# Optimization experiments

Hardware: AMD Instinct MI355X
Metric: run time of the kernel (lower is better)

## Reference

```python
import jax, jax.numpy as jnp
import numpy as np

EPS = 1e-5
K = 5

def _bn(x, g, b):
    # BatchNorm1d in training mode: biased batch statistics
    mu = jnp.mean(x, axis=0)
    var = jnp.mean((x - mu) ** 2, axis=0)
    return (x - mu) * jax.lax.rsqrt(var + EPS) * g + b

def setup_inputs():
    key = jax.random.key(0)
    ks = jax.random.split(key, 16)
    N, M, D, F = 16384, 8192, 512, 2048
    s = 0.02
    return dict(
        src=jax.random.normal(ks[0], (N, D), jnp.float32),
        anchor_2=jax.random.normal(ks[1], (M, D), jnp.float32),
        W_dim=jax.random.normal(ks[2], (D, D), jnp.float32) * s,
        b_dim=jnp.zeros((D,), jnp.float32),
        W_fus=jax.random.normal(ks[3], (2 * D, D), jnp.float32) * s,
        b_fus=jnp.zeros((D,), jnp.float32),
        W_e1=jax.random.normal(ks[4], (D, F), jnp.float32) * s,
        b_e1=jnp.zeros((F,), jnp.float32),
        W_e2=jax.random.normal(ks[5], (F, D), jnp.float32) * s,
        b_e2=jnp.zeros((D,), jnp.float32),
        g1=jnp.ones((D,), jnp.float32), bt1=jnp.zeros((D,), jnp.float32),
        g2=jnp.ones((D,), jnp.float32), bt2=jnp.zeros((D,), jnp.float32),
        W_d=jax.random.normal(ks[6], (D, D), jnp.float32) * s,
        b_d=jnp.zeros((D,), jnp.float32),
        g_d=jnp.ones((D,), jnp.float32), bt_d=jnp.zeros((D,), jnp.float32),
    )

def reference(src, anchor_2, W_dim, b_dim, W_fus, b_fus, W_e1, b_e1, W_e2, b_e2,
              g1, bt1, g2, bt2, W_d, b_d, g_d, bt_d):
    # kNN in Euclidean metric (sklearn NearestNeighbors): squared distances suffice
    # d2[n,m] = ||src_n||^2 - 2 src_n . a_m + ||a_m||^2   -> [N, M]
    d2 = (jnp.sum(src * src, axis=1, keepdims=True)
          - 2.0 * (src @ anchor_2.T)
          + jnp.sum(anchor_2 * anchor_2, axis=1)[None, :])
    _, idx = jax.lax.top_k(-d2, K)                      # [N, K] nearest anchors
    neigh = jnp.mean(anchor_2[idx], axis=1)             # gather + mean -> [N, D]
    a_map = neigh @ W_dim + b_dim                       # linear_dim
    comb = jnp.concatenate([src, a_map], axis=1) @ W_fus + b_fus
    comb = _bn(comb, g1, bt1)                           # norm1
    # encoder MLP (dropout is identity in eval)
    t = jnp.tanh(comb @ W_e1 + b_e1) @ W_e2 + b_e2
    comb = _bn(comb + t, g2, bt2)                       # residual + norm2
    out = jnp.tanh(_bn(comb @ W_d + b_d, g_d, bt_d))    # decoder
    return out
```

## Files before the change

### kernel.cpp

```cpp
#include <hip/hip_runtime.h>
#include <math.h>

#define N_ROWS 16384
#define M_ANCH 8192
#define DDIM   512
#define FDIM   2048
#define KNN    5
#define BN_EPS 1e-5f
#define CHUNK  8192
#define SEED   1024
#define CAND_MAX 256
#define MARGIN 6.0f
#define QSCALE 28.0f
#define TWO_INV_S2 (2.0f / (QSCALE * QSCALE))

typedef _Float16 f16;
typedef _Float16 f16x8 __attribute__((ext_vector_type(8)));
typedef _Float16 f16x4 __attribute__((ext_vector_type(4)));
typedef float f32x4 __attribute__((ext_vector_type(4)));
typedef int   i32x4 __attribute__((ext_vector_type(4)));

__device__ __forceinline__ void async_copy16(const void* g, void* l) {
    __builtin_amdgcn_global_load_lds(
        (const __attribute__((address_space(1))) void*)g,
        (__attribute__((address_space(3))) void*)l, 16, 0, 0);
}

__device__ __forceinline__ bool kless(float k1, int i1, float k2, int i2) {
    return (k1 < k2) || (k1 == k2 && i1 < i2);
}

__device__ __forceinline__ void insert5(float (&bk)[KNN], int (&bi)[KNN], float key, int id) {
    if (!kless(key, id, bk[4], bi[4])) return;
    bool c3 = kless(key, id, bk[3], bi[3]);
    bool c2 = kless(key, id, bk[2], bi[2]);
    bool c1 = kless(key, id, bk[1], bi[1]);
    bool c0 = kless(key, id, bk[0], bi[0]);
    bk[4] = c3 ? bk[3] : key;                  bi[4] = c3 ? bi[3] : id;
    bk[3] = c3 ? (c2 ? bk[2] : key) : bk[3];   bi[3] = c3 ? (c2 ? bi[2] : id) : bi[3];
    bk[2] = c2 ? (c1 ? bk[1] : key) : bk[2];   bi[2] = c2 ? (c1 ? bi[1] : id) : bi[2];
    bk[1] = c1 ? (c0 ? bk[0] : key) : bk[1];   bi[1] = c1 ? (c0 ? bi[0] : id) : bi[1];
    bk[0] = c0 ? key : bk[0];                  bi[0] = c0 ? id : bi[0];
}

__global__ void zero_kernel(float* p, int n) {
    int i = blockIdx.x * blockDim.x + threadIdx.x;
    if (i < n) p[i] = 0.f;
}

__global__ __launch_bounds__(256) void quant_i8_kernel(const float* __restrict__ X,
                                                       unsigned int* __restrict__ Y, int n4) {
    int i = blockIdx.x * 256 + threadIdx.x;
    if (i >= n4) return;
    float4 v = ((const float4*)X)[i];
    int a = (int)rintf(v.x * QSCALE); a = a > 127 ? 127 : (a < -127 ? -127 : a);
    int b = (int)rintf(v.y * QSCALE); b = b > 127 ? 127 : (b < -127 ? -127 : b);
    int c = (int)rintf(v.z * QSCALE); c = c > 127 ? 127 : (c < -127 ? -127 : c);
    int d = (int)rintf(v.w * QSCALE); d = d > 127 ? 127 : (d < -127 ? -127 : d);
    Y[i] = (unsigned int)(a & 255) | ((unsigned int)(b & 255) << 8)
         | ((unsigned int)(c & 255) << 16) | ((unsigned int)(d & 255) << 24);
}

__global__ __launch_bounds__(256) void anchor_norm_kernel(const float* __restrict__ a,
                                                          float* __restrict__ norm_a) {
    int wave = threadIdx.x >> 6, lane = threadIdx.x & 63;
    int row = blockIdx.x * 4 + wave;
    const float4* ar = (const float4*)(a + (size_t)row * DDIM);
    float4 v1 = ar[lane * 2];
    float4 v2 = ar[lane * 2 + 1];
    float s = v1.x*v1.x + v1.y*v1.y + v1.z*v1.z + v1.w*v1.w
            + v2.x*v2.x + v2.y*v2.y + v2.z*v2.z + v2.w*v2.w;
    for (int off = 32; off; off >>= 1) s += __shfl_xor(s, off, 64);
    if (lane == 0) norm_a[row] = s;
}

template<int COLLECT>
__global__ __launch_bounds__(256) void gemm_i8(
    const char* __restrict__ A, const char* __restrict__ B,
    const float* __restrict__ norm, const float* __restrict__ thr,
    int* __restrict__ cnt, int* __restrict__ cand_i, float* __restrict__ cand_n,
    int idofs, float* __restrict__ C, int Ncols)
{
    __shared__ char As[2][128 * 64];
    __shared__ char Bs[2][128 * 64];
    const int t = threadIdx.x;
    const int w = t >> 6, l = t & 63;
    const int m0 = blockIdx.y * 128, n0 = blockIdx.x * 128;
    const int wm = (w & 1) * 64, wn = (w >> 1) * 64;

    i32x4 acc[4][4];
    #pragma unroll
    for (int i = 0; i < 4; ++i)
        #pragma unroll
        for (int j = 0; j < 4; ++j) acc[i][j] = (i32x4){0, 0, 0, 0};

    const int srow = l >> 2;
    const int gq = ((l & 3) - (srow >> 1)) & 3;
    const int skoff = gq * 16;
    const int sqf = (((l >> 4) + (((l & 15) >> 1) & 3)) & 3) * 16;

    auto STAGE = [&](int buf, int kt) {
        int k0 = kt * 64;
        #pragma unroll
        for (int s = 0; s < 2; ++s) {
            int grp = w * 2 + s;
            int row = grp * 16 + srow;
            async_copy16(A + (size_t)(m0 + row) * DDIM + k0 + skoff,
                         &As[buf][grp * 1024 + l * 16]);
            async_copy16(B + (size_t)(n0 + row) * DDIM + k0 + skoff,
                         &Bs[buf][grp * 1024 + l * 16]);
        }
    };

    STAGE(0, 0);
    __syncthreads();

    for (int kt = 0; kt < 8; ++kt) {
        int cur = kt & 1;
        if (kt < 7) STAGE(cur ^ 1, kt + 1);
        i32x4 af[4], bf[4];
        #pragma unroll
        for (int i = 0; i < 4; ++i)
            af[i] = *(const i32x4*)&As[cur][(wm + i * 16 + (l & 15)) * 64 + sqf];
        #pragma unroll
        for (int j = 0; j < 4; ++j)
            bf[j] = *(const i32x4*)&Bs[cur][(wn + j * 16 + (l & 15)) * 64 + sqf];
        #pragma unroll
        for (int i = 0; i < 4; ++i)
            #pragma unroll
            for (int j = 0; j < 4; ++j)
                acc[i][j] = __builtin_amdgcn_mfma_i32_16x16x64_i8(af[i], bf[j], acc[i][j], 0, 0, 0);
        __syncthreads();
    }

    float nj[4];
    #pragma unroll
    for (int j = 0; j < 4; ++j) nj[j] = norm[n0 + wn + j * 16 + (l & 15)];

    if (COLLECT) {
        float thr4[4][4];
        #pragma unroll
        for (int i = 0; i < 4; ++i) {
            float4 tv = *(const float4*)&thr[m0 + wm + i * 16 + (l >> 4) * 4];
            thr4[i][0] = tv.x; thr4[i][1] = tv.y; thr4[i][2] = tv.z; thr4[i][3] = tv.w;
        }
        #pragma unroll
        for (int i = 0; i < 4; ++i)
            #pragma unroll
            for (int j = 0; j < 4; ++j)
                #pragma unroll
                for (int r = 0; r < 4; ++r) {
                    float key = nj[j] - TWO_INV_S2 * (float)acc[i][j][r];
                    if (key < thr4[i][r]) {
                        int row = m0 + wm + i * 16 + (l >> 4) * 4 + r;
                        int pos = atomicAdd(&cnt[row], 1);
                        if (pos < CAND_MAX) {
                            cand_i[(size_t)row * CAND_MAX + pos] =
                                idofs + n0 + wn + j * 16 + (l & 15);
                            cand_n[(size_t)row * CAND_MAX + pos] = nj[j];
                        }
                    }
                }
    } else {
        #pragma unroll
        for (int i = 0; i < 4; ++i)
            #pragma unroll
            for (int j = 0; j < 4; ++j)
                #pragma unroll
                for (int r = 0; r < 4; ++r) {
                    int m = m0 + wm + i * 16 + (l >> 4) * 4 + r;
                    int n = n0 + wn + j * 16 + (l & 15);
                    C[(size_t)m * Ncols + n] = nj[j] - TWO_INV_S2 * (float)acc[i][j][r];
                }
    }
}

__global__ __launch_bounds__(256) void topk_scan_kernel(
    const float* __restrict__ g, const float* __restrict__ norm_a,
    float* __restrict__ thrbuf, int* __restrict__ cnt,
    int* __restrict__ cand_i, float* __restrict__ cand_n)
{
    int row = blockIdx.x * 4 + (threadIdx.x >> 6);
    int lane = threadIdx.x & 63;
    const float* grow = g + (size_t)row * SEED;
    float4 v0 = *(const float4*)(grow + lane * 4);
    float4 v1 = *(const float4*)(grow + 256 + lane * 4);
    float4 v2 = *(const float4*)(grow + 512 + lane * 4);
    float4 v3 = *(const float4*)(grow + 768 + lane * 4);
    float bk[KNN]; int bi[KNN];
    #pragma unroll
    for (int q = 0; q < KNN; ++q) { bk[q] = 3.0e38f; bi[q] = 0x7fffffff; }
    int c = lane * 4;
    insert5(bk, bi, v0.x, c);       insert5(bk, bi, v0.y, c + 1);
    insert5(bk, bi, v0.z, c + 2);   insert5(bk, bi, v0.w, c + 3);
    insert5(bk, bi, v1.x, c + 256); insert5(bk, bi, v1.y, c + 257);
    insert5(bk, bi, v1.z, c + 258); insert5(bk, bi, v1.w, c + 259);
    insert5(bk, bi, v2.x, c + 512); insert5(bk, bi, v2.y, c + 513);
    insert5(bk, bi, v2.z, c + 514); insert5(bk, bi, v2.w, c + 515);
    insert5(bk, bi, v3.x, c + 768); insert5(bk, bi, v3.y, c + 769);
    insert5(bk, bi, v3.z, c + 770); insert5(bk, bi, v3.w, c + 771);
    for (int off = 32; off >= 1; off >>= 1) {
        float ok[KNN]; int oi[KNN];
        #pragma unroll
        for (int q = 0; q < KNN; ++q) {
            ok[q] = __shfl_xor(bk[q], off, 64);
            oi[q] = __shfl_xor(bi[q], off, 64);
        }
        #pragma unroll
        for (int q = 0; q < KNN; ++q) insert5(bk, bi, ok[q], oi[q]);
    }
    float thr = bk[4] + MARGIN;
    if (lane == 0) thrbuf[row] = thr;
    int* rci = cand_i + (size_t)row * CAND_MAX;
    float* rcn = cand_n + (size_t)row * CAND_MAX;
    #define PUSH(v, id) if ((v) < thr) { int pos = atomicAdd(&cnt[row], 1); \
                                         if (pos < CAND_MAX) { rci[pos] = (id); \
                                         rcn[pos] = norm_a[(id)]; } }
    PUSH(v0.x, c)       PUSH(v0.y, c + 1)   PUSH(v0.z, c + 2)   PUSH(v0.w, c + 3)
    PUSH(v1.x, c + 256) PUSH(v1.y, c + 257) PUSH(v1.z, c + 258) PUSH(v1.w, c + 259)
    PUSH(v2.x, c + 512) PUSH(v2.y, c + 513) PUSH(v2.z, c + 514) PUSH(v2.w, c + 515)
    PUSH(v3.x, c + 768) PUSH(v3.y, c + 769) PUSH(v3.z, c + 770) PUSH(v3.w, c + 771)
    #undef PUSH
}

__global__ __launch_bounds__(256) void rescore_kernel(
    const float* __restrict__ src, const float* __restrict__ anchor,
    const int* __restrict__ cnt, const int* __restrict__ cand_i,
    const float* __restrict__ cand_n, float* __restrict__ neigh)
{
    __shared__ float lb[4][2][DDIM];
    int wv = threadIdx.x >> 6, lane = threadIdx.x & 63;
    int row = blockIdx.x * 4 + wv;
    const float4* sp = (const float4*)(src + (size_t)row * DDIM);
    float4 s0 = sp[lane * 2], s1 = sp[lane * 2 + 1];
    int c = cnt[row]; if (c > CAND_MAX) c = CAND_MAX;
    const int* ci = cand_i + (size_t)row * CAND_MAX;
    const float* cn = cand_n + (size_t)row * CAND_MAX;

    float bk[KNN]; int bi[KNN];
    #pragma unroll
    for (int q = 0; q < KNN; ++q) { bk[q] = 3.0e38f; bi[q] = 0x7fffffff; }

    auto PREF = [&](int buf, int id) {
        const float* gp = anchor + (size_t)id * DDIM;
        async_copy16(gp + lane * 4, &lb[wv][buf][lane * 4]);
        async_copy16(gp + 256 + lane * 4, &lb[wv][buf][256 + lane * 4]);
    };

    int   id_c = ci[0];          float n_c = cn[0];
    int   id_n = ci[1];          float n_n = cn[1];
    PREF(0, id_c);
    PREF(1, id_n);

    for (int p = 0; p < c; ++p) {
        int id_f = 0; float n_f = 0.f;
        if (p + 2 < c) { id_f = ci[p + 2]; n_f = cn[p + 2]; }
        asm volatile("s_waitcnt vmcnt(4)" ::: "memory");
        const float* bc = &lb[wv][p & 1][0];
        float4 a0 = *(const float4*)&bc[lane * 8];
        float4 a1 = *(const float4*)&bc[lane * 8 + 4];
        float d = s0.x*a0.x + s0.y*a0.y + s0.z*a0.z + s0.w*a0.w
                + s1.x*a1.x + s1.y*a1.y + s1.z*a1.z + s1.w*a1.w;
        #pragma unroll
        for (int off = 32; off; off >>= 1) d += __shfl_xor(d, off, 64);
        insert5(bk, bi, n_c - 2.f * d, id_c);
        if (p + 2 < c) PREF(p & 1, id_f);
        id_c = id_n; n_c = n_n;
        id_n = id_f; n_n = n_f;
    }

    const float4* a0 = (const float4*)(anchor + (size_t)bi[0] * DDIM);
    const float4* a1 = (const float4*)(anchor + (size_t)bi[1] * DDIM);
    const float4* a2 = (const float4*)(anchor + (size_t)bi[2] * DDIM);
    const float4* a3 = (const float4*)(anchor + (size_t)bi[3] * DDIM);
    const float4* a4 = (const float4*)(anchor + (size_t)bi[4] * DDIM);
    float4* np = (float4*)(neigh + (size_t)row * DDIM);
    #pragma unroll
    for (int p = 0; p < 2; ++p) {
        int c4 = lane + 64 * p;
        float4 v0 = a0[c4], v1 = a1[c4], v2 = a2[c4], v3 = a3[c4], v4 = a4[c4];
        float4 o;
        o.x = (v0.x + v1.x + v2.x + v3.x + v4.x) * 0.2f;
        o.y = (v0.y + v1.y + v2.y + v3.y + v4.y) * 0.2f;
        o.z = (v0.z + v1.z + v2.z + v3.z + v4.z) * 0.2f;
        o.w = (v0.w + v1.w + v2.w + v3.w + v4.w) * 0.2f;
        np[c4] = o;
    }
}

template<int ADDC0, int TANH, int K>
__global__ __launch_bounds__(256) void gemm_split_nt(
    const float* __restrict__ A, const f16* __restrict__ Bw,
    const float* __restrict__ bias, const float* __restrict__ C0,
    float* __restrict__ C, int Ncols)
{
    __shared__ f16 Ah[128 * 32];
    __shared__ f16 Al[128 * 32];
    __shared__ f16 Bh[128 * 32];
    __shared__ f16 Bl[128 * 32];
    const int t = threadIdx.x;
    const int w = t >> 6, l = t & 63;
    const int m0 = blockIdx.y * 128, n0 = blockIdx.x * 128;
    const int wm = (w & 1) * 64, wn = (w >> 1) * 64;
    const int K2 = 2 * K;

    f32x4 acc[4][4];
    #pragma unroll
    for (int i = 0; i < 4; ++i)
        #pragma unroll
        for (int j = 0; j < 4; ++j) acc[i][j] = (f32x4){0.f, 0.f, 0.f, 0.f};

    const int ar = t >> 1;
    const int ac = (t & 1) * 16;
    const int arq = (ar >> 1) & 3;
    const int s0 = (((t & 1) * 2 + 0 + arq) & 3) * 8;
    const int s1 = (((t & 1) * 2 + 1 + arq) & 3) * 8;
    const int srow = l >> 2;
    const int gq = ((l & 3) - (srow >> 1)) & 3;
    const int skoff = gq * 8;
    const int sqf = (((l >> 4) + (((l & 15) >> 1) & 3)) & 3) * 8;

    for (int k0 = 0; k0 < K; k0 += 32) {
        __syncthreads();
        #pragma unroll
        for (int s = 0; s < 2; ++s) {
            int grp = w * 2 + s;
            int row = grp * 16 + srow;
            const f16* bp = Bw + (size_t)(n0 + row) * K2 + k0 + skoff;
            async_copy16(bp, Bh + grp * 512 + l * 8);
            async_copy16(bp + K, Bl + grp * 512 + l * 8);
        }
        {
            const float* ap = A + (size_t)(m0 + ar) * K + k0 + ac;
            float xs[16];
            *(float4*)&xs[0]  = *(const float4*)ap;
            *(float4*)&xs[4]  = *(const float4*)(ap + 4);
            *(float4*)&xs[8]  = *(const float4*)(ap + 8);
            *(float4*)&xs[12] = *(const float4*)(ap + 12);
            f16x8 h0, h1, lo0, lo1;
            #pragma unroll
            for (int e = 0; e < 8; ++e) {
                f16 hh = (f16)xs[e];
                h0[e] = hh; lo0[e] = (f16)(xs[e] - (float)hh);
                f16 hh2 = (f16)xs[8 + e];
                h1[e] = hh2; lo1[e] = (f16)(xs[8 + e] - (float)hh2);
            }
            *(f16x8*)&Ah[ar * 32 + s0] = h0;  *(f16x8*)&Ah[ar * 32 + s1] = h1;
            *(f16x8*)&Al[ar * 32 + s0] = lo0; *(f16x8*)&Al[ar * 32 + s1] = lo1;
        }
        __syncthreads();
        f16x8 afh[4], afl[4], bfh[4], bfl[4];
        #pragma unroll
        for (int i = 0; i < 4; ++i) {
            int base = (wm + i * 16 + (l & 15)) * 32 + sqf;
            afh[i] = *(const f16x8*)(Ah + base);
            afl[i] = *(const f16x8*)(Al + base);
        }
        #pragma unroll
        for (int j = 0; j < 4; ++j) {
            int base = (wn + j * 16 + (l & 15)) * 32 + sqf;
            bfh[j] = *(const f16x8*)(Bh + base);
            bfl[j] = *(const f16x8*)(Bl + base);
        }
        #pragma unroll
        for (int i = 0; i < 4; ++i)
            #pragma unroll
            for (int j = 0; j < 4; ++j) {
                acc[i][j] = __builtin_amdgcn_mfma_f32_16x16x32_f16(afh[i], bfh[j], acc[i][j], 0, 0, 0);
                acc[i][j] = __builtin_amdgcn_mfma_f32_16x16x32_f16(afl[i], bfh[j], acc[i][j], 0, 0, 0);
                acc[i][j] = __builtin_amdgcn_mfma_f32_16x16x32_f16(afh[i], bfl[j], acc[i][j], 0, 0, 0);
            }
    }
    float bv[4];
    #pragma unroll
    for (int j = 0; j < 4; ++j)
        bv[j] = bias ? bias[n0 + wn + j * 16 + (l & 15)] : 0.f;
    #pragma unroll
    for (int i = 0; i < 4; ++i)
        #pragma unroll
        for (int j = 0; j < 4; ++j)
            #pragma unroll
            for (int r = 0; r < 4; ++r) {
                int m = m0 + wm + i * 16 + (l >> 4) * 4 + r;
                int n = n0 + wn + j * 16 + (l & 15);
                float v = acc[i][j][r] + bv[j];
                if (ADDC0) v += C0[(size_t)m * Ncols + n];
                if (TANH)  v = tanhf(v);
                C[(size_t)m * Ncols + n] = v;
            }
}

__global__ __launch_bounds__(256) void wsplit_kernel(const float* __restrict__ W,
                                                     f16* __restrict__ Wt,
                                                     int K, int N)
{
    __shared__ float tile[64][65];
    const int t = threadIdx.x;
    const int kb = blockIdx.y * 64, nb = blockIdx.x * 64;
    #pragma unroll
    for (int i = 0; i < 4; ++i) {
        int r = (t >> 4) + i * 16;
        int c = (t & 15) * 4;
        *(float4*)&tile[r][c] = *(const float4*)&W[(size_t)(kb + r) * N + nb + c];
    }
    __syncthreads();
    const int r2 = t >> 2;
    const int kc = (t & 3) * 16;
    f16x8 h0, h1, lo0, lo1;
    #pragma unroll
    for (int e = 0; e < 8; ++e) {
        float x = tile[kc + e][r2];
        f16 hh = (f16)x; h0[e] = hh; lo0[e] = (f16)(x - (float)hh);
        float y = tile[kc + 8 + e][r2];
        f16 hh2 = (f16)y; h1[e] = hh2; lo1[e] = (f16)(y - (float)hh2);
    }
    f16* base = Wt + (size_t)(nb + r2) * 2 * K + kb + kc;
    *(f16x8*)base = h0; *(f16x8*)(base + 8) = h1;
    *(f16x8*)(base + K) = lo0; *(f16x8*)(base + K + 8) = lo1;
}

__global__ __launch_bounds__(256) void bcomb_kernel(const float* __restrict__ b_dim,
                                                    const float* __restrict__ W_fus2,
                                                    const float* __restrict__ b_fus,
                                                    float* __restrict__ b_comb)
{
    int n = blockIdx.x * 256 + threadIdx.x;
    if (n >= DDIM) return;
    float s = b_fus[n];
    for (int k = 0; k < DDIM; ++k) s += b_dim[k] * W_fus2[(size_t)k * DDIM + n];
    b_comb[n] = s;
}

template<int ACT>
__global__ __launch_bounds__(256) void gemm_kernel(
    const float* __restrict__ A, int K1,
    const float* __restrict__ A2, int K2,
    const float* __restrict__ B, const float* __restrict__ bias,
    float* __restrict__ C, int Ncols)
{
    __shared__ float As[16][132];
    __shared__ float Bs[16][128];
    const int t = threadIdx.x;
    const int n0 = blockIdx.x * 128;
    const int m0 = blockIdx.y * 128;
    const int ty = t >> 4, tx = t & 15;
    const int K = K1 + K2;

    float acc[8][8];
    #pragma unroll
    for (int i = 0; i < 8; ++i)
        #pragma unroll
        for (int j = 0; j < 8; ++j) acc[i][j] = 0.f;

    const int ar = t >> 1;
    const int akc = (t & 1) * 8;
    const int bkr = t >> 4;
    const int bc = (t & 15) * 8;

    for (int k0 = 0; k0 < K; k0 += 16) {
        int kk = k0 + akc;
        float4 v0, v1;
        if (kk < K1) {
            const float* p = A + (size_t)(m0 + ar) * K1 + kk;
            v0 = *(const float4*)p; v1 = *(const float4*)(p + 4);
        } else {
            const float* p = A2 + (size_t)(m0 + ar) * K2 + (kk - K1);
            v0 = *(const float4*)p; v1 = *(const float4*)(p + 4);
        }
        const float* bp = B + (size_t)(k0 + bkr) * Ncols + n0 + bc;
        float4 w0 = *(const float4*)bp, w1 = *(const float4*)(bp + 4);
        __syncthreads();
        As[akc+0][ar] = v0.x; As[akc+1][ar] = v0.y; As[akc+2][ar] = v0.z; As[akc+3][ar] = v0.w;
        As[akc+4][ar] = v1.x; As[akc+5][ar] = v1.y; As[akc+6][ar] = v1.z; As[akc+7][ar] = v1.w;
        *(float4*)&Bs[bkr][bc] = w0; *(float4*)&Bs[bkr][bc + 4] = w1;
        __syncthreads();
        #pragma unroll
        for (int k = 0; k < 16; ++k) {
            float a[8], b[8];
            *(float4*)&a[0] = *(const float4*)&As[k][ty * 8];
            *(float4*)&a[4] = *(const float4*)&As[k][ty * 8 + 4];
            *(float4*)&b[0] = *(const float4*)&Bs[k][tx * 4];
            *(float4*)&b[4] = *(const float4*)&Bs[k][64 + tx * 4];
            #pragma unroll
            for (int i = 0; i < 8; ++i)
                #pragma unroll
                for (int j = 0; j < 8; ++j) acc[i][j] += a[i] * b[j];
        }
    }
    float4 bv0 = *(const float4*)(bias + n0 + tx * 4);
    float4 bv1 = *(const float4*)(bias + n0 + 64 + tx * 4);
    #pragma unroll
    for (int i = 0; i < 8; ++i) {
        int row = m0 + ty * 8 + i;
        float4 o0, o1;
        o0.x = acc[i][0] + bv0.x; o0.y = acc[i][1] + bv0.y;
        o0.z = acc[i][2] + bv0.z; o0.w = acc[i][3] + bv0.w;
        o1.x = acc[i][4] + bv1.x; o1.y = acc[i][5] + bv1.y;
        o1.z = acc[i][6] + bv1.z; o1.w = acc[i][7] + bv1.w;
        if (ACT == 1) {
            o0.x = tanhf(o0.x); o0.y = tanhf(o0.y); o0.z = tanhf(o0.z); o0.w = tanhf(o0.w);
            o1.x = tanhf(o1.x); o1.y = tanhf(o1.y); o1.z = tanhf(o1.z); o1.w = tanhf(o1.w);
        }
        *(float4*)(C + (size_t)row * Ncols + n0 + tx * 4) = o0;
        *(float4*)(C + (size_t)row * Ncols + n0 + 64 + tx * 4) = o1;
    }
}

__global__ __launch_bounds__(256) void bn_stats_kernel(const float* __restrict__ X,
                                                       float* __restrict__ sums)
{
    __shared__ float red[8][64];
    int lane = threadIdx.x & 63;
    int rl = threadIdx.x >> 6;
    int c = blockIdx.x * 64 + lane;
    int chunk = N_ROWS / gridDim.y;
    int rbeg = blockIdx.y * chunk;
    float s = 0.f, s2 = 0.f;
    for (int r = rbeg + rl; r < rbeg + chunk; r += 4) {
        float v = X[(size_t)r * DDIM + c];
        s += v; s2 += v * v;
    }
    red[rl][lane] = s; red[4 + rl][lane] = s2;
    __syncthreads();
    if (threadIdx.x < 64) {
        float ts = red[0][lane] + red[1][lane] + red[2][lane] + red[3][lane];
        float t2 = red[4][lane] + red[5][lane] + red[6][lane] + red[7][lane];
        atomicAdd(&sums[c], ts);
        atomicAdd(&sums[DDIM + c], t2);
    }
}

template<int TANH>
__global__ __launch_bounds__(256) void bn_apply_kernel(
    const float* __restrict__ X, float* __restrict__ Y,
    const float* __restrict__ sums, const float* __restrict__ g,
    const float* __restrict__ b, float invN)
{
    size_t i = (size_t)blockIdx.x * 256 + threadIdx.x;
    int cg = (int)(i % (DDIM / 4));
    int c = cg * 4;
    float4 x = ((const float4*)X)[i];
    float4 sm = *(const float4*)(sums + c);
    float4 sq = *(const float4*)(sums + DDIM + c);
    float4 gv = *(const float4*)(g + c);
    float4 bv = *(const float4*)(b + c);
    float m, var, rs;
    m = sm.x * invN; var = sq.x * invN - m * m; rs = rsqrtf(var + BN_EPS);
    x.x = (x.x - m) * rs * gv.x + bv.x;
    m = sm.y * invN; var = sq.y * invN - m * m; rs = rsqrtf(var + BN_EPS);
    x.y = (x.y - m) * rs * gv.y + bv.y;
    m = sm.z * invN; var = sq.z * invN - m * m; rs = rsqrtf(var + BN_EPS);
    x.z = (x.z - m) * rs * gv.z + bv.z;
    m = sm.w * invN; var = sq.w * invN - m * m; rs = rsqrtf(var + BN_EPS);
    x.w = (x.w - m) * rs * gv.w + bv.w;
    if (TANH) { x.x = tanhf(x.x); x.y = tanhf(x.y); x.z = tanhf(x.z); x.w = tanhf(x.w); }
    ((float4*)Y)[i] = x;
}

extern "C" void kernel_launch(void* const* d_in, const int* in_sizes, int n_in,
                              void* d_out, int out_size, void* d_ws, size_t ws_size,
                              hipStream_t stream)
{
    const float* src   = (const float*)d_in[0];
    const float* anc   = (const float*)d_in[1];
    const float* W_dim = (const float*)d_in[2];
    const float* b_dim = (const float*)d_in[3];
    const float* W_fus = (const float*)d_in[4];
    const float* b_fus = (const float*)d_in[5];
    const float* W_e1  = (const float*)d_in[6];
    const float* b_e1  = (const float*)d_in[7];
    const float* W_e2  = (const float*)d_in[8];
    const float* b_e2  = (const float*)d_in[9];
    const float* g1    = (const float*)d_in[10];
    const float* bt1   = (const float*)d_in[11];
    const float* g2    = (const float*)d_in[12];
    const float* bt2   = (const float*)d_in[13];
    const float* W_d   = (const float*)d_in[14];
    const float* b_d   = (const float*)d_in[15];
    const float* g_d   = (const float*)d_in[16];
    const float* bt_d  = (const float*)d_in[17];
    float* out = (float*)d_out;

    float* ws = (float*)d_ws;
    float* score  = ws;
    float* bufA   = ws + 16777216;
    char*  src2q  = (char*)(ws + 25165824);
    char*  anc2q  = (char*)(ws + 37748736);
    f16*   wbase  = (f16*)(ws + 25165824);
    f16*   Wt_fus1  = wbase;
    f16*   Wt_comb2 = wbase + 524288;
    f16*   Wt_e1    = wbase + 1048576;
    f16*   Wt_e2    = wbase + 3145728;
    f16*   Wt_d     = wbase + 5242880;
    float* cand_n   = ws + 29360128;
    float* W_comb2  = ws + 44040192;
    float* norm_a   = ws + 44302336;
    float* sums1    = ws + 44310528;
    float* sums2    = sums1 + 1024;
    float* sums3    = sums2 + 1024;
    float* zeros512 = ws + 44313600;
    float* b_comb   = ws + 44314112;
    float* thrbuf   = ws + 44478464;
    int*   cnt      = (int*)(ws + 44494848);
    int*   cand_i   = (int*)(ws + 48705536);

    const float invN = 1.0f / (float)N_ROWS;
    float* hbuf = score;

    zero_kernel<<<dim3(14), 256, 0, stream>>>(sums1, 3584);
    zero_kernel<<<dim3(64), 256, 0, stream>>>((float*)cnt, 16384);
    quant_i8_kernel<<<dim3(N_ROWS * DDIM / 1024), 256, 0, stream>>>(
        src, (unsigned int*)src2q, N_ROWS * DDIM / 4);
    quant_i8_kernel<<<dim3(M_ANCH * DDIM / 1024), 256, 0, stream>>>(
        anc, (unsigned int*)anc2q, M_ANCH * DDIM / 4);
    anchor_norm_kernel<<<dim3(M_ANCH / 4), 256, 0, stream>>>(anc, norm_a);

    gemm_i8<0><<<dim3(SEED / 128, N_ROWS / 128), 256, 0, stream>>>(
        src2q, anc2q, norm_a, nullptr, nullptr, nullptr, nullptr, 0, score, SEED);
    topk_scan_kernel<<<dim3(N_ROWS / 4), 256, 0, stream>>>(
        score, norm_a, thrbuf, cnt, cand_i, cand_n);
    gemm_i8<1><<<dim3((M_ANCH - SEED) / 128, N_ROWS / 128), 256, 0, stream>>>(
        src2q, anc2q + (size_t)SEED * DDIM, norm_a + SEED, thrbuf,
        cnt, cand_i, cand_n, SEED, nullptr, 0);
    rescore_kernel<<<dim3(N_ROWS / 4), 256, 0, stream>>>(
        src, anc, cnt, cand_i, cand_n, bufA);

    wsplit_kernel<<<dim3(DDIM / 64, DDIM / 64), 256, 0, stream>>>(W_fus, Wt_fus1, DDIM, DDIM);
    wsplit_kernel<<<dim3(FDIM / 64, DDIM / 64), 256, 0, stream>>>(W_e1, Wt_e1, DDIM, FDIM);
    wsplit_kernel<<<dim3(DDIM / 64, FDIM / 64), 256, 0, stream>>>(W_e2, Wt_e2, FDIM, DDIM);
    wsplit_kernel<<<dim3(DDIM / 64, DDIM / 64), 256, 0, stream>>>(W_d, Wt_d, DDIM, DDIM);
    gemm_kernel<0><<<dim3(4, 4), 256, 0, stream>>>(
        W_dim, DDIM, nullptr, 0, W_fus + DDIM * DDIM, zeros512, W_comb2, DDIM);
    bcomb_kernel<<<dim3(2), 256, 0, stream>>>(b_dim, W_fus + DDIM * DDIM, b_fus, b_comb);
    wsplit_kernel<<<dim3(DDIM / 64, DDIM / 64), 256, 0, stream>>>(W_comb2, Wt_comb2, DDIM, DDIM);

    gemm_split_nt<0, 0, DDIM><<<dim3(DDIM / 128, N_ROWS / 128), 256, 0, stream>>>(
        src, Wt_fus1, b_comb, nullptr, out, DDIM);
    gemm_split_nt<1, 0, DDIM><<<dim3(DDIM / 128, N_ROWS / 128), 256, 0, stream>>>(
        bufA, Wt_comb2, nullptr, out, out, DDIM);
    bn_stats_kernel<<<dim3(DDIM / 64, 16), 256, 0, stream>>>(out, sums1);
    bn_apply_kernel<0><<<dim3(8192), 256, 0, stream>>>(out, out, sums1, g1, bt1, invN);

    for (int r0 = 0; r0 < N_ROWS; r0 += CHUNK) {
        gemm_split_nt<0, 1, DDIM><<<dim3(FDIM / 128, CHUNK / 128), 256, 0, stream>>>(
            out + (size_t)r0 * DDIM, Wt_e1, b_e1, nullptr, hbuf, FDIM);
        gemm_split_nt<1, 0, FDIM><<<dim3(DDIM / 128, CHUNK / 128), 256, 0, stream>>>(
            hbuf, Wt_e2, b_e2, out + (size_t)r0 * DDIM, bufA + (size_t)r0 * DDIM,
            DDIM);
    }
    bn_stats_kernel<<<dim3(DDIM / 64, 16), 256, 0, stream>>>(bufA, sums2);
    bn_apply_kernel<0><<<dim3(8192), 256, 0, stream>>>(bufA, bufA, sums2, g2, bt2, invN);

    gemm_split_nt<0, 0, DDIM><<<dim3(DDIM / 128, N_ROWS / 128), 256, 0, stream>>>(
        bufA, Wt_d, b_d, nullptr, out, DDIM);
    bn_stats_kernel<<<dim3(DDIM / 64, 16), 256, 0, stream>>>(out, sums3);
    bn_apply_kernel<1><<<dim3(8192), 256, 0, stream>>>(out, out, sums3, g_d, bt_d, invN);
}
```

Before: 1.644 ms.

## Split kNN rescore across two waves per row and double-buffer split GEMM

The rescore kernel now assigns two wavefronts to each row, each scoring alternate candidates, then merges their top-5 lists through shared memory before one wave gathers and averages the neighbours. The split-fp16 GEMM gains double-buffered LDS tiles, so the next K-slice's A and B loads overlap the MFMA work on the current slice and one barrier per iteration is removed. The aim is more parallelism in the latency-bound candidate loop and better overlap of memory with compute in the GEMMs. The cost is doubled LDS use in the GEMM, which may lower occupancy, plus an extra block-level sync and an idle half of the waves during the rescore gather.

Result: slower. 1.690 ms (+2.8%).

```diff
diff --git a/kernel.cpp b/kernel.cpp
--- a/kernel.cpp
+++ b/kernel.cpp
@@ -229,13 +229,17 @@
     const float* __restrict__ cand_n, float* __restrict__ neigh)
 {
     __shared__ float lb[4][2][DDIM];
+    __shared__ float mgk[4][KNN];
+    __shared__ int   mgi[4][KNN];
     int wv = threadIdx.x >> 6, lane = threadIdx.x & 63;
-    int row = blockIdx.x * 4 + wv;
+    int row = blockIdx.x * 2 + (wv >> 1);
+    int sub = wv & 1;
     const float4* sp = (const float4*)(src + (size_t)row * DDIM);
     float4 s0 = sp[lane * 2], s1 = sp[lane * 2 + 1];
     int c = cnt[row]; if (c > CAND_MAX) c = CAND_MAX;
     const int* ci = cand_i + (size_t)row * CAND_MAX;
     const float* cn = cand_n + (size_t)row * CAND_MAX;
+    int nw = (c - sub + 1) >> 1;
 
     float bk[KNN]; int bi[KNN];
     #pragma unroll
@@ -243,48 +247,59 @@
 
     auto PREF = [&](int buf, int id) {
         const float* gp = anchor + (size_t)id * DDIM;
-        async_copy16(gp + lane * 4, &lb[wv][buf][lane * 4]);
-        async_copy16(gp + 256 + lane * 4, &lb[wv][buf][256 + lane * 4]);
+        async_copy16(gp + lane * 8,     &lb[wv][buf][lane * 4]);
+        async_copy16(gp + lane * 8 + 4, &lb[wv][buf][256 + lane * 4]);
     };
 
-    int   id_c = ci[0];          float n_c = cn[0];
-    int   id_n = ci[1];          float n_n = cn[1];
+    int   id_c = ci[sub];       float n_c = cn[sub];
+    int   id_n = ci[sub + 2];   float n_n = cn[sub + 2];
     PREF(0, id_c);
     PREF(1, id_n);
 
-    for (int p = 0; p < c; ++p) {
+    for (int t = 0; t < nw; ++t) {
         int id_f = 0; float n_f = 0.f;
-        if (p + 2 < c) { id_f = ci[p + 2]; n_f = cn[p + 2]; }
-        asm volatile("s_waitcnt vmcnt(4)" ::: "memory");
-        const float* bc = &lb[wv][p & 1][0];
-        float4 a0 = *(const float4*)&bc[lane * 8];
-        float4 a1 = *(const float4*)&bc[lane * 8 + 4];
+        if (t + 2 < nw) { id_f = ci[sub + 2 * (t + 2)]; n_f = cn[sub + 2 * (t + 2)]; }
+        if (t + 2 < nw)      asm volatile("s_waitcnt vmcnt(4)" ::: "memory");
+        else if (t + 1 < nw) asm volatile("s_waitcnt vmcnt(2)" ::: "memory");
+        else                 asm volatile("s_waitcnt vmcnt(0)" ::: "memory");
+        const float* bc = &lb[wv][t & 1][0];
+        float4 a0 = *(const float4*)&bc[lane * 4];
+        float4 a1 = *(const float4*)&bc[256 + lane * 4];
         float d = s0.x*a0.x + s0.y*a0.y + s0.z*a0.z + s0.w*a0.w
                 + s1.x*a1.x + s1.y*a1.y + s1.z*a1.z + s1.w*a1.w;
         #pragma unroll
         for (int off = 32; off; off >>= 1) d += __shfl_xor(d, off, 64);
         insert5(bk, bi, n_c - 2.f * d, id_c);
-        if (p + 2 < c) PREF(p & 1, id_f);
+        if (t + 2 < nw) PREF(t & 1, id_f);
         id_c = id_n; n_c = n_n;
         id_n = id_f; n_n = n_f;
     }
 
-    const float4* a0 = (const float4*)(anchor + (size_t)bi[0] * DDIM);
-    const float4* a1 = (const float4*)(anchor + (size_t)bi[1] * DDIM);
-    const float4* a2 = (const float4*)(anchor + (size_t)bi[2] * DDIM);
-    const float4* a3 = (const float4*)(anchor + (size_t)bi[3] * DDIM);
-    const float4* a4 = (const float4*)(anchor + (size_t)bi[4] * DDIM);
-    float4* np = (float4*)(neigh + (size_t)row * DDIM);
-    #pragma unroll
-    for (int p = 0; p < 2; ++p) {
-        int c4 = lane + 64 * p;
-        float4 v0 = a0[c4], v1 = a1[c4], v2 = a2[c4], v3 = a3[c4], v4 = a4[c4];
-        float4 o;
-        o.x = (v0.x + v1.x + v2.x + v3.x + v4.x) * 0.2f;
-        o.y = (v0.y + v1.y + v2.y + v3.y + v4.y) * 0.2f;
-        o.z = (v0.z + v1.z + v2.z + v3.z + v4.z) * 0.2f;
-        o.w = (v0.w + v1.w + v2.w + v3.w + v4.w) * 0.2f;
-        np[c4] = o;
+    if (lane == 0) {
+        #pragma unroll
+        for (int q = 0; q < KNN; ++q) { mgk[wv][q] = bk[q]; mgi[wv][q] = bi[q]; }
+    }
+    __syncthreads();
+    if (sub == 0) {
+        #pragma unroll
+        for (int q = 0; q < KNN; ++q) insert5(bk, bi, mgk[wv ^ 1][q], mgi[wv ^ 1][q]);
+        const float4* a0 = (const float4*)(anchor + (size_t)bi[0] * DDIM);
+        const float4* a1 = (const float4*)(anchor + (size_t)bi[1] * DDIM);
+        const float4* a2 = (const float4*)(anchor + (size_t)bi[2] * DDIM);
+        const float4* a3 = (const float4*)(anchor + (size_t)bi[3] * DDIM);
+        const float4* a4 = (const float4*)(anchor + (size_t)bi[4] * DDIM);
+        float4* np = (float4*)(neigh + (size_t)row * DDIM);
+        #pragma unroll
+        for (int p = 0; p < 2; ++p) {
+            int c4 = lane + 64 * p;
+            float4 v0 = a0[c4], v1 = a1[c4], v2 = a2[c4], v3 = a3[c4], v4 = a4[c4];
+            float4 o;
+            o.x = (v0.x + v1.x + v2.x + v3.x + v4.x) * 0.2f;
+            o.y = (v0.y + v1.y + v2.y + v3.y + v4.y) * 0.2f;
+            o.z = (v0.z + v1.z + v2.z + v3.z + v4.z) * 0.2f;
+            o.w = (v0.w + v1.w + v2.w + v3.w + v4.w) * 0.2f;
+            np[c4] = o;
+        }
     }
 }
 
@@ -294,15 +309,16 @@
     const float* __restrict__ bias, const float* __restrict__ C0,
     float* __restrict__ C, int Ncols)
 {
-    __shared__ f16 Ah[128 * 32];
-    __shared__ f16 Al[128 * 32];
-    __shared__ f16 Bh[128 * 32];
-    __shared__ f16 Bl[128 * 32];
+    __shared__ f16 Ah[2][128 * 32];
+    __shared__ f16 Al[2][128 * 32];
+    __shared__ f16 Bh[2][128 * 32];
+    __shared__ f16 Bl[2][128 * 32];
     const int t = threadIdx.x;
     const int w = t >> 6, l = t & 63;
     const int m0 = blockIdx.y * 128, n0 = blockIdx.x * 128;
     const int wm = (w & 1) * 64, wn = (w >> 1) * 64;
     const int K2 = 2 * K;
+    const int NK = K / 32;
 
     f32x4 acc[4][4];
     #pragma unroll
@@ -320,47 +336,62 @@
     const int skoff = gq * 8;
     const int sqf = (((l >> 4) + (((l & 15) >> 1) & 3)) & 3) * 8;
 
-    for (int k0 = 0; k0 < K; k0 += 32) {
-        __syncthreads();
+    auto STAGE_B = [&](int buf, int kt) {
+        int k0 = kt * 32;
         #pragma unroll
         for (int s = 0; s < 2; ++s) {
             int grp = w * 2 + s;
             int row = grp * 16 + srow;
             const f16* bp = Bw + (size_t)(n0 + row) * K2 + k0 + skoff;
-            async_copy16(bp, Bh + grp * 512 + l * 8);
-            async_copy16(bp + K, Bl + grp * 512 + l * 8);
-        }
-        {
-            const float* ap = A + (size_t)(m0 + ar) * K + k0 + ac;
-            float xs[16];
-            *(float4*)&xs[0]  = *(const float4*)ap;
-            *(float4*)&xs[4]  = *(const float4*)(ap + 4);
-            *(float4*)&xs[8]  = *(const float4*)(ap + 8);
-            *(float4*)&xs[12] = *(const float4*)(ap + 12);
-            f16x8 h0, h1, lo0, lo1;
-            #pragma unroll
-            for (int e = 0; e < 8; ++e) {
-                f16 hh = (f16)xs[e];
-                h0[e] = hh; lo0[e] = (f16)(xs[e] - (float)hh);
-                f16 hh2 = (f16)xs[8 + e];
-                h1[e] = hh2; lo1[e] = (f16)(xs[8 + e] - (float)hh2);
-            }
-            *(f16x8*)&Ah[ar * 32 + s0] = h0;  *(f16x8*)&Ah[ar * 32 + s1] = h1;
-            *(f16x8*)&Al[ar * 32 + s0] = lo0; *(f16x8*)&Al[ar * 32 + s1] = lo1;
-        }
-        __syncthreads();
+            async_copy16(bp, &Bh[buf][grp * 512 + l * 8]);
+            async_copy16(bp + K, &Bl[buf][grp * 512 + l * 8]);
+        }
+    };
+    auto A_LOAD = [&](int kt, float4& x0, float4& x1, float4& x2, float4& x3) {
+        const float* ap = A + (size_t)(m0 + ar) * K + kt * 32 + ac;
+        x0 = *(const float4*)ap;       x1 = *(const float4*)(ap + 4);
+        x2 = *(const float4*)(ap + 8); x3 = *(const float4*)(ap + 12);
+    };
+    auto A_WRITE = [&](int buf, float4 x0, float4 x1, float4 x2, float4 x3) {
+        float xs[16];
+        *(float4*)&xs[0] = x0; *(float4*)&xs[4] = x1;
+        *(float4*)&xs[8] = x2; *(float4*)&xs[12] = x3;
+        f16x8 h0, h1, lo0, lo1;
+        #pragma unroll
+        for (int e = 0; e < 8; ++e) {
+            f16 hh = (f16)xs[e];
+            h0[e] = hh; lo0[e] = (f16)(xs[e] - (float)hh);
+            f16 hh2 = (f16)xs[8 + e];
+            h1[e] = hh2; lo1[e] = (f16)(xs[8 + e] - (float)hh2);
+        }
+        *(f16x8*)&Ah[buf][ar * 32 + s0] = h0;  *(f16x8*)&Ah[buf][ar * 32 + s1] = h1;
+        *(f16x8*)&Al[buf][ar * 32 + s0] = lo0; *(f16x8*)&Al[buf][ar * 32 + s1] = lo1;
+    };
+
+    float4 x0, x1, x2, x3;
+    A_LOAD(0, x0, x1, x2, x3);
+    STAGE_B(0, 0);
+    A_WRITE(0, x0, x1, x2, x3);
+    __syncthreads();
+
+    for (int kt = 0; kt < NK; ++kt) {
+        int cur = kt & 1;
+        if (kt + 1 < NK) {
+            STAGE_B(cur ^ 1, kt + 1);
+            A_LOAD(kt + 1, x0, x1, x2, x3);
+        }
         f16x8 afh[4], afl[4], bfh[4], bfl[4];
         #pragma unroll
         for (int i = 0; i < 4; ++i) {
             int base = (wm + i * 16 + (l & 15)) * 32 + sqf;
-            afh[i] = *(const f16x8*)(Ah + base);
-            afl[i] = *(const f16x8*)(Al + base);
+            afh[i] = *(const f16x8*)&Ah[cur][base];
+            afl[i] = *(const f16x8*)&Al[cur][base];
         }
         #pragma unroll
         for (int j = 0; j < 4; ++j) {
             int base = (wn + j * 16 + (l & 15)) * 32 + sqf;
-            bfh[j] = *(const f16x8*)(Bh + base);
-            bfl[j] = *(const f16x8*)(Bl + base);
+            bfh[j] = *(const f16x8*)&Bh[cur][base];
+            bfl[j] = *(const f16x8*)&Bl[cur][base];
         }
         #pragma unroll
         for (int i = 0; i < 4; ++i)
@@ -370,6 +401,10 @@
                 acc[i][j] = __builtin_amdgcn_mfma_f32_16x16x32_f16(afl[i], bfh[j], acc[i][j], 0, 0, 0);
                 acc[i][j] = __builtin_amdgcn_mfma_f32_16x16x32_f16(afh[i], bfl[j], acc[i][j], 0, 0, 0);
             }
+        if (kt + 1 < NK) {
+            A_WRITE(cur ^ 1, x0, x1, x2, x3);
+            __syncthreads();
+        }
     }
     float bv[4];
     #pragma unroll
@@ -622,7 +657,7 @@
     gemm_i8<1><<<dim3((M_ANCH - SEED) / 128, N_ROWS / 128), 256, 0, stream>>>(
         src2q, anc2q + (size_t)SEED * DDIM, norm_a + SEED, thrbuf,
         cnt, cand_i, cand_n, SEED, nullptr, 0);
-    rescore_kernel<<<dim3(N_ROWS / 4), 256, 0, stream>>>(
+    rescore_kernel<<<dim3(N_ROWS / 2), 256, 0, stream>>>(
         src, anc, cnt, cand_i, cand_n, bufA);
 
     wsplit_kernel<<<dim3(DDIM / 64, DDIM / 64), 256, 0, stream>>>(W_fus, Wt_fus1, DDIM, DDIM);
```

## Pre-split activations to f16 hi/lo and double-buffer GEMM tiles via async LDS copies

Applied to the files above, without the earlier changes.

Adds a rowsplit kernel that converts fp32 activations into a row-major f16 hi/lo layout before each dense GEMM. The GEMM now loads both A and B tiles with async global-to-LDS copies into double-buffered shared memory, which removes per-tile in-register conversion and lets the next tile's load overlap the current tile's MFMAs. The cost is extra passes over memory to write the split activations, and twice the LDS per block, which may lower occupancy. The rescore prefetch layout is also changed to contiguous 8-float lanes, and workspace offsets are moved.

Result: slower. 1.711 ms (+4.0%).

```diff
diff --git a/kernel.cpp b/kernel.cpp
--- a/kernel.cpp
+++ b/kernel.cpp
@@ -59,6 +59,24 @@
     int d = (int)rintf(v.w * QSCALE); d = d > 127 ? 127 : (d < -127 ? -127 : d);
     Y[i] = (unsigned int)(a & 255) | ((unsigned int)(b & 255) << 8)
          | ((unsigned int)(c & 255) << 16) | ((unsigned int)(d & 255) << 24);
+}
+
+__global__ __launch_bounds__(256) void rowsplit_kernel(const float* __restrict__ X,
+                                                       f16* __restrict__ Y,
+                                                       int n4, int log_k4) {
+    int i4 = blockIdx.x * 256 + threadIdx.x;
+    if (i4 >= n4) return;
+    int K4 = 1 << log_k4;
+    int row = i4 >> log_k4;
+    int kc = (i4 & (K4 - 1)) * 4;
+    float4 v = ((const float4*)X)[i4];
+    f16x4 h, lo;
+    h.x = (f16)v.x; h.y = (f16)v.y; h.z = (f16)v.z; h.w = (f16)v.w;
+    lo.x = (f16)(v.x - (float)h.x); lo.y = (f16)(v.y - (float)h.y);
+    lo.z = (f16)(v.z - (float)h.z); lo.w = (f16)(v.w - (float)h.w);
+    f16* base = Y + (size_t)row * (K4 * 8) + kc;
+    *(f16x4*)base = h;
+    *(f16x4*)(base + K4 * 4) = lo;
 }
 
 __global__ __launch_bounds__(256) void anchor_norm_kernel(const float* __restrict__ a,
@@ -243,8 +261,8 @@
 
     auto PREF = [&](int buf, int id) {
         const float* gp = anchor + (size_t)id * DDIM;
-        async_copy16(gp + lane * 4, &lb[wv][buf][lane * 4]);
-        async_copy16(gp + 256 + lane * 4, &lb[wv][buf][256 + lane * 4]);
+        async_copy16(gp + lane * 8,     &lb[wv][buf][lane * 4]);
+        async_copy16(gp + lane * 8 + 4, &lb[wv][buf][256 + lane * 4]);
     };
 
     int   id_c = ci[0];          float n_c = cn[0];
@@ -257,8 +275,8 @@
         if (p + 2 < c) { id_f = ci[p + 2]; n_f = cn[p + 2]; }
         asm volatile("s_waitcnt vmcnt(4)" ::: "memory");
         const float* bc = &lb[wv][p & 1][0];
-        float4 a0 = *(const float4*)&bc[lane * 8];
-        float4 a1 = *(const float4*)&bc[lane * 8 + 4];
+        float4 a0 = *(const float4*)&bc[lane * 4];
+        float4 a1 = *(const float4*)&bc[256 + lane * 4];
         float d = s0.x*a0.x + s0.y*a0.y + s0.z*a0.z + s0.w*a0.w
                 + s1.x*a1.x + s1.y*a1.y + s1.z*a1.z + s1.w*a1.w;
         #pragma unroll
@@ -289,20 +307,21 @@
 }
 
 template<int ADDC0, int TANH, int K>
-__global__ __launch_bounds__(256) void gemm_split_nt(
-    const float* __restrict__ A, const f16* __restrict__ Bw,
+__global__ __launch_bounds__(256) void gemm_f16hl(
+    const f16* __restrict__ Aw, const f16* __restrict__ Bw,
     const float* __restrict__ bias, const float* __restrict__ C0,
     float* __restrict__ C, int Ncols)
 {
-    __shared__ f16 Ah[128 * 32];
-    __shared__ f16 Al[128 * 32];
-    __shared__ f16 Bh[128 * 32];
-    __shared__ f16 Bl[128 * 32];
+    __shared__ f16 Ah[2][128 * 32];
+    __shared__ f16 Al[2][128 * 32];
+    __shared__ f16 Bh[2][128 * 32];
+    __shared__ f16 Bl[2][128 * 32];
     const int t = threadIdx.x;
     const int w = t >> 6, l = t & 63;
     const int m0 = blockIdx.y * 128, n0 = blockIdx.x * 128;
     const int wm = (w & 1) * 64, wn = (w >> 1) * 64;
     const int K2 = 2 * K;
+    const int NK = K / 32;
 
     f32x4 acc[4][4];
     #pragma unroll
@@ -310,57 +329,44 @@
         #pragma unroll
         for (int j = 0; j < 4; ++j) acc[i][j] = (f32x4){0.f, 0.f, 0.f, 0.f};
 
-    const int ar = t >> 1;
-    const int ac = (t & 1) * 16;
-    const int arq = (ar >> 1) & 3;
-    const int s0 = (((t & 1) * 2 + 0 + arq) & 3) * 8;
-    const int s1 = (((t & 1) * 2 + 1 + arq) & 3) * 8;
     const int srow = l >> 2;
     const int gq = ((l & 3) - (srow >> 1)) & 3;
     const int skoff = gq * 8;
     const int sqf = (((l >> 4) + (((l & 15) >> 1) & 3)) & 3) * 8;
 
-    for (int k0 = 0; k0 < K; k0 += 32) {
-        __syncthreads();
+    auto STAGE = [&](int buf, int kt) {
+        int k0 = kt * 32;
         #pragma unroll
         for (int s = 0; s < 2; ++s) {
             int grp = w * 2 + s;
             int row = grp * 16 + srow;
+            const f16* ap = Aw + (size_t)(m0 + row) * K2 + k0 + skoff;
+            async_copy16(ap,     &Ah[buf][grp * 512 + l * 8]);
+            async_copy16(ap + K, &Al[buf][grp * 512 + l * 8]);
             const f16* bp = Bw + (size_t)(n0 + row) * K2 + k0 + skoff;
-            async_copy16(bp, Bh + grp * 512 + l * 8);
-            async_copy16(bp + K, Bl + grp * 512 + l * 8);
-        }
-        {
-            const float* ap = A + (size_t)(m0 + ar) * K + k0 + ac;
-            float xs[16];
-            *(float4*)&xs[0]  = *(const float4*)ap;
-            *(float4*)&xs[4]  = *(const float4*)(ap + 4);
-            *(float4*)&xs[8]  = *(const float4*)(ap + 8);
-            *(float4*)&xs[12] = *(const float4*)(ap + 12);
-            f16x8 h0, h1, lo0, lo1;
-            #pragma unroll
-            for (int e = 0; e < 8; ++e) {
-                f16 hh = (f16)xs[e];
-                h0[e] = hh; lo0[e] = (f16)(xs[e] - (float)hh);
-                f16 hh2 = (f16)xs[8 + e];
-                h1[e] = hh2; lo1[e] = (f16)(xs[8 + e] - (float)hh2);
-            }
-            *(f16x8*)&Ah[ar * 32 + s0] = h0;  *(f16x8*)&Ah[ar * 32 + s1] = h1;
-            *(f16x8*)&Al[ar * 32 + s0] = lo0; *(f16x8*)&Al[ar * 32 + s1] = lo1;
-        }
-        __syncthreads();
+            async_copy16(bp,     &Bh[buf][grp * 512 + l * 8]);
+            async_copy16(bp + K, &Bl[buf][grp * 512 + l * 8]);
+        }
+    };
+
+    STAGE(0, 0);
+    __syncthreads();
+
+    for (int kt = 0; kt < NK; ++kt) {
+        int cur = kt & 1;
+        if (kt + 1 < NK) STAGE(cur ^ 1, kt + 1);
         f16x8 afh[4], afl[4], bfh[4], bfl[4];
         #pragma unroll
         for (int i = 0; i < 4; ++i) {
             int base = (wm + i * 16 + (l & 15)) * 32 + sqf;
-            afh[i] = *(const f16x8*)(Ah + base);
-            afl[i] = *(const f16x8*)(Al + base);
+            afh[i] = *(const f16x8*)&Ah[cur][base];
+            afl[i] = *(const f16x8*)&Al[cur][base];
         }
         #pragma unroll
         for (int j = 0; j < 4; ++j) {
             int base = (wn + j * 16 + (l & 15)) * 32 + sqf;
-            bfh[j] = *(const f16x8*)(Bh + base);
-            bfl[j] = *(const f16x8*)(Bl + base);
+            bfh[j] = *(const f16x8*)&Bh[cur][base];
+            bfl[j] = *(const f16x8*)&Bl[cur][base];
         }
         #pragma unroll
         for (int i = 0; i < 4; ++i)
@@ -370,6 +376,7 @@
                 acc[i][j] = __builtin_amdgcn_mfma_f32_16x16x32_f16(afl[i], bfh[j], acc[i][j], 0, 0, 0);
                 acc[i][j] = __builtin_amdgcn_mfma_f32_16x16x32_f16(afh[i], bfl[j], acc[i][j], 0, 0, 0);
             }
+        __syncthreads();
     }
     float bv[4];
     #pragma unroll
@@ -592,22 +599,24 @@
     f16*   Wt_e1    = wbase + 1048576;
     f16*   Wt_e2    = wbase + 3145728;
     f16*   Wt_d     = wbase + 5242880;
+    f16*   aslot    = (f16*)(ws + 28049408);
+    f16*   h_h      = (f16*)(ws + 28049408);
+    f16*   combh    = (f16*)(ws + 44826624);
     float* cand_n   = ws + 29360128;
     float* W_comb2  = ws + 44040192;
     float* norm_a   = ws + 44302336;
-    float* sums1    = ws + 44310528;
-    float* sums2    = sums1 + 1024;
-    float* sums3    = sums2 + 1024;
-    float* zeros512 = ws + 44313600;
-    float* b_comb   = ws + 44314112;
     float* thrbuf   = ws + 44478464;
     int*   cnt      = (int*)(ws + 44494848);
     int*   cand_i   = (int*)(ws + 48705536);
+    float* sums1    = ws + 49020928;
+    float* sums2    = sums1 + 1024;
+    float* sums3    = sums2 + 1024;
+    float* zeros512 = ws + 49024000;
+    float* b_comb   = ws + 49024512;
 
     const float invN = 1.0f / (float)N_ROWS;
     float* hbuf = score;
 
-    zero_kernel<<<dim3(14), 256, 0, stream>>>(sums1, 3584);
     zero_kernel<<<dim3(64), 256, 0, stream>>>((float*)cnt, 16384);
     quant_i8_kernel<<<dim3(N_ROWS * DDIM / 1024), 256, 0, stream>>>(
         src, (unsigned int*)src2q, N_ROWS * DDIM / 4);
@@ -625,6 +634,8 @@
     rescore_kernel<<<dim3(N_ROWS / 4), 256, 0, stream>>>(
         src, anc, cnt, cand_i, cand_n, bufA);
 
+    zero_kernel<<<dim3(14), 256, 0, stream>>>(sums1, 3584);
+
     wsplit_kernel<<<dim3(DDIM / 64, DDIM / 64), 256, 0, stream>>>(W_fus, Wt_fus1, DDIM, DDIM);
     wsplit_kernel<<<dim3(FDIM / 64, DDIM / 64), 256, 0, stream>>>(W_e1, Wt_e1, DDIM, FDIM);
     wsplit_kernel<<<dim3(DDIM / 64, FDIM / 64), 256, 0, stream>>>(W_e2, Wt_e2, FDIM, DDIM);
@@ -634,25 +645,35 @@
     bcomb_kernel<<<dim3(2), 256, 0, stream>>>(b_dim, W_fus + DDIM * DDIM, b_fus, b_comb);
     wsplit_kernel<<<dim3(DDIM / 64, DDIM / 64), 256, 0, stream>>>(W_comb2, Wt_comb2, DDIM, DDIM);
 
-    gemm_split_nt<0, 0, DDIM><<<dim3(DDIM / 128, N_ROWS / 128), 256, 0, stream>>>(
-        src, Wt_fus1, b_comb, nullptr, out, DDIM);
-    gemm_split_nt<1, 0, DDIM><<<dim3(DDIM / 128, N_ROWS / 128), 256, 0, stream>>>(
-        bufA, Wt_comb2, nullptr, out, out, DDIM);
+    rowsplit_kernel<<<dim3(N_ROWS * DDIM / 1024), 256, 0, stream>>>(
+        src, aslot, N_ROWS * DDIM / 4, 7);
+    gemm_f16hl<0, 0, DDIM><<<dim3(DDIM / 128, N_ROWS / 128), 256, 0, stream>>>(
+        aslot, Wt_fus1, b_comb, nullptr, out, DDIM);
+    rowsplit_kernel<<<dim3(N_ROWS * DDIM / 1024), 256, 0, stream>>>(
+        bufA, aslot, N_ROWS * DDIM / 4, 7);
+    gemm_f16hl<1, 0, DDIM><<<dim3(DDIM / 128, N_ROWS / 128), 256, 0, stream>>>(
+        aslot, Wt_comb2, nullptr, out, out, DDIM);
     bn_stats_kernel<<<dim3(DDIM / 64, 16), 256, 0, stream>>>(out, sums1);
     bn_apply_kernel<0><<<dim3(8192), 256, 0, stream>>>(out, out, sums1, g1, bt1, invN);
 
     for (int r0 = 0; r0 < N_ROWS; r0 += CHUNK) {
-        gemm_split_nt<0, 1, DDIM><<<dim3(FDIM / 128, CHUNK / 128), 256, 0, stream>>>(
-            out + (size_t)r0 * DDIM, Wt_e1, b_e1, nullptr, hbuf, FDIM);
-        gemm_split_nt<1, 0, FDIM><<<dim3(DDIM / 128, CHUNK / 128), 256, 0, stream>>>(
-            hbuf, Wt_e2, b_e2, out + (size_t)r0 * DDIM, bufA + (size_t)r0 * DDIM,
+        rowsplit_kernel<<<dim3(CHUNK * DDIM / 1024), 256, 0, stream>>>(
+            out + (size_t)r0 * DDIM, combh, CHUNK * DDIM / 4, 7);
+        gemm_f16hl<0, 1, DDIM><<<dim3(FDIM / 128, CHUNK / 128), 256, 0, stream>>>(
+            combh, Wt_e1, b_e1, nullptr, hbuf, FDIM);
+        rowsplit_kernel<<<dim3(CHUNK * FDIM / 1024), 256, 0, stream>>>(
+            hbuf, h_h, CHUNK * FDIM / 4, 9);
+        gemm_f16hl<1, 0, FDIM><<<dim3(DDIM / 128, CHUNK / 128), 256, 0, stream>>>(
+            h_h, Wt_e2, b_e2, out + (size_t)r0 * DDIM, bufA + (size_t)r0 * DDIM,
             DDIM);
     }
     bn_stats_kernel<<<dim3(DDIM / 64, 16), 256, 0, stream>>>(bufA, sums2);
     bn_apply_kernel<0><<<dim3(8192), 256, 0, stream>>>(bufA, bufA, sums2, g2, bt2, invN);
 
-    gemm_split_nt<0, 0, DDIM><<<dim3(DDIM / 128, N_ROWS / 128), 256, 0, stream>>>(
-        bufA, Wt_d, b_d, nullptr, out, DDIM);
+    rowsplit_kernel<<<dim3(N_ROWS * DDIM / 1024), 256, 0, stream>>>(
+        bufA, aslot, N_ROWS * DDIM / 4, 7);
+    gemm_f16hl<0, 0, DDIM><<<dim3(DDIM / 128, N_ROWS / 128), 256, 0, stream>>>(
+        aslot, Wt_d, b_d, nullptr, out, DDIM);
     bn_stats_kernel<<<dim3(DDIM / 64, 16), 256, 0, stream>>>(out, sums3);
     bn_apply_kernel<1><<<dim3(8192), 256, 0, stream>>>(out, out, sums3, g_d, bt_d, invN);
 }
```
